# Kernel tuning notes

Measured on AMD Instinct MI355X. Metric: run time of the kernel, lower is better.

Reference implementation:

```python
import jax, jax.numpy as jnp
import numpy as np


def _maxpool2(x):
    # 2x2 max pool, stride 2, NCHW
    return jax.lax.reduce_window(x, -jnp.inf, jax.lax.max, (1, 1, 2, 2), (1, 1, 2, 2), 'VALID')


def _up2(x):
    # bilinear upsample x2 with align_corners=True (matches nn.Upsample), NCHW, separable
    def rs(a, axis):
        n = a.shape[axis]
        out = 2 * n
        c = jnp.arange(out) * ((n - 1) / (out - 1))
        i0 = jnp.floor(c).astype(jnp.int32)
        i1 = jnp.minimum(i0 + 1, n - 1)
        w = (c - i0).astype(a.dtype)
        lo = jnp.take(a, i0, axis=axis)
        hi = jnp.take(a, i1, axis=axis)
        shp = [1] * a.ndim
        shp[axis] = out
        w = w.reshape(shp)
        return lo * (1 - w) + hi * w
    return rs(rs(x, 2), 3)


def _conv_experts(x, w, b):
    # x [B,Cin,H,W], w [E,Cout,Cin,3,3], b [E,Cout] -> [E,B,Cout,H,W]
    def one(we, be):
        y = jax.lax.conv_general_dilated(x, we, (1, 1), 'SAME',
                                         dimension_numbers=('NCHW', 'OIHW', 'NCHW'))
        return jax.nn.relu(y + be[None, :, None, None])
    return jax.vmap(one)(w, b)


def _moe(x, cw, cb, gw, gb, nw, nb, eps, k):
    # noisy top-k gate (create_gate) + fused gated expert sum (eval_gate)
    B = x.shape[0]
    xf = x.reshape(B, -1)
    g = xf @ gw + gb                      # [B,E]
    noise = jax.nn.softplus(xf @ nw + nb)
    g = g + eps[None, :] * noise          # shared per-expert gaussian noise * per-sample scale
    E = g.shape[1]
    if E > 2:
        _, idx = jax.lax.top_k(g.sum(axis=0), k)   # top-k experts by batch-summed gate
        mask = jnp.zeros((E,), bool).at[idx].set(True)
        g = jnp.where(mask[None, :], g, 0.0)       # zero BEFORE softmax, as in the original
    gate = jax.nn.softmax(g, axis=-1)
    y = _conv_experts(x, cw, cb)          # [E,B,C,H,W]
    # collapses the original experts x batch python double-loop into one contraction
    return jnp.einsum('ebchw,be->bchw', y, gate)


def setup_inputs():
    key = jax.random.key(0)
    keys = iter(jax.random.split(key, 40))
    def rn(shape, scale=1.0):
        return jax.random.normal(next(keys), shape, jnp.float32) * scale
    B, W, E = 2048, 10, 4
    inp = {'x': rn((B, 1, 28, 28))}
    conv_shapes = [(E, W, 1, 3, 3), (E, W, W, 3, 3), (E, 2 * W, W, 3, 3),
                   (E, W, 3 * W, 3, 3), (E, W, 2 * W, 3, 3)]
    gate_in = [784, 1960, 490, 5880, 15680]
    for i in range(5):
        inp[f'cw{i+1}'] = rn(conv_shapes[i], 0.1)
        inp[f'cb{i+1}'] = rn((E, conv_shapes[i][1]), 0.1)
        inp[f'gw{i+1}'] = rn((gate_in[i], E), 0.02)
        inp[f'gb{i+1}'] = rn((E,), 0.02)
        inp[f'nw{i+1}'] = rn((gate_in[i], E), 0.02)
        inp[f'nb{i+1}'] = rn((E,), 0.02)
        inp[f'eps{i+1}'] = rn((E,), 1.0)   # N(mu=0, sigma=1) gate noise, fixed for determinism
    inp['wlast'] = rn((1, W, 1, 1), 0.1)
    inp['blast'] = rn((1,), 0.1)
    inp['k'] = 2
    return inp


def reference(x, cw1, cb1, gw1, gb1, nw1, nb1, eps1,
              cw2, cb2, gw2, gb2, nw2, nb2, eps2,
              cw3, cb3, gw3, gb3, nw3, nb3, eps3,
              cw4, cb4, gw4, gb4, nw4, nb4, eps4,
              cw5, cb5, gw5, gb5, nw5, nb5, eps5,
              wlast, blast, k):
    conv1 = _moe(x, cw1, cb1, gw1, gb1, nw1, nb1, eps1, k)        # [B,10,28,28]
    h = _maxpool2(conv1)                                          # [B,10,14,14]
    conv2 = _moe(h, cw2, cb2, gw2, gb2, nw2, nb2, eps2, k)        # [B,10,14,14]
    h = _maxpool2(conv2)                                          # [B,10,7,7]
    conv3 = _moe(h, cw3, cb3, gw3, gb3, nw3, nb3, eps3, k)        # [B,20,7,7]
    h = jnp.concatenate([_up2(conv3), conv2], axis=1)             # [B,30,14,14]
    h = _moe(h, cw4, cb4, gw4, gb4, nw4, nb4, eps4, k)            # [B,10,14,14]
    h = jnp.concatenate([_up2(h), conv1], axis=1)                 # [B,20,28,28]
    h = _moe(h, cw5, cb5, gw5, gb5, nw5, nb5, eps5, k)            # [B,10,28,28]
    out = jnp.einsum('bchw,oc->bohw', h, wlast[:, :, 0, 0]) + blast[None, :, None, None]
    return out
```

## Files before the change

### kernel.cpp

```cpp
#include <hip/hip_runtime.h>
#include <hip/hip_bf16.h>
#include <math.h>


constexpr int BATCH = 2048;

constexpr size_t PADF    = 1024;
constexpr size_t F_CONV1 = (size_t)BATCH * 10 * 784;
constexpr size_t F_XPAD  = (size_t)BATCH * 784;
constexpr size_t F_P1    = (size_t)BATCH * 10 * 196;
constexpr size_t F_CONV2 = F_P1;
constexpr size_t F_P2    = (size_t)BATCH * 10 * 49;
constexpr size_t F_CONV3 = (size_t)BATCH * 20 * 49;
constexpr size_t F_UP3   = (size_t)BATCH * 20 * 196;
constexpr size_t F_M4    = F_P1;
constexpr size_t F_UP4   = F_CONV1;

constexpr size_t O_CONV1 = PADF;
constexpr size_t O_Z2    = O_CONV1 + F_CONV1 + PADF;
constexpr size_t O_XPAD  = O_Z2;
constexpr size_t O_P1    = O_XPAD + F_XPAD + PADF;
constexpr size_t O_CONV2 = O_P1 + F_P1 + PADF;
constexpr size_t O_P2    = O_CONV2 + F_CONV2 + PADF;
constexpr size_t O_CONV3 = O_P2 + F_P2 + PADF;
constexpr size_t O_UP3   = O_CONV3 + F_CONV3 + PADF;
constexpr size_t O_M4    = O_UP3 + F_UP3 + PADF;
constexpr size_t O_UP4   = O_Z2;
constexpr size_t O_GRAW  = O_M4 + F_M4 + PADF;
constexpr size_t O_CS    = O_GRAW + 5 * (size_t)BATCH * 4;
constexpr size_t WS_FLOATS = O_CS + 5 * 64 + PADF;

__device__ __forceinline__ float softplusf(float z) {
    return fmaxf(z, 0.0f) + log1pf(expf(-fabsf(z)));
}

__device__ __forceinline__ float4 ld4(const float* p) {
    return *(const float4*)p;
}

constexpr int cdivc(int a, int b) { return (a + b - 1) / b; }
constexpr int pb4(int H, int W) {
    return cdivc(BATCH * ((H + 3) / 4) * W, 256);
}

template <int C1HW, int C2HW>
__global__ __launch_bounds__(256) void gate_block_v4(
    const float* __restrict__ x1, const float* __restrict__ x2,
    const float* __restrict__ gw, const float* __restrict__ gb,
    const float* __restrict__ nw, const float* __restrict__ nb,
    const float* __restrict__ eps,
    float* __restrict__ graw)
{
    constexpr int DV = (C1HW + C2HW) / 4;
    const int b0  = blockIdx.x * 2;
    const int tid = threadIdx.x;

    float ga[2][4] = {}, na[2][4] = {};

    for (int g = tid; g < DV; g += 256) {
        const int d = g * 4;
        float4 xv[2];
        #pragma unroll
        for (int ss = 0; ss < 2; ++ss) {
            const int b = b0 + ss;
            if constexpr (C2HW > 0) {
                xv[ss] = (d < C1HW) ? ld4(x1 + (size_t)b * C1HW + d)
                                    : ld4(x2 + (size_t)b * C2HW + (d - C1HW));
            } else {
                xv[ss] = ld4(x1 + (size_t)b * C1HW + d);
            }
        }
        #pragma unroll
        for (int j = 0; j < 4; ++j) {
            const float4 gv = ((const float4*)gw)[d + j];
            const float4 nv = ((const float4*)nw)[d + j];
            #pragma unroll
            for (int ss = 0; ss < 2; ++ss) {
                const float val = (&xv[ss].x)[j];
                ga[ss][0] = fmaf(val, gv.x, ga[ss][0]);
                ga[ss][1] = fmaf(val, gv.y, ga[ss][1]);
                ga[ss][2] = fmaf(val, gv.z, ga[ss][2]);
                ga[ss][3] = fmaf(val, gv.w, ga[ss][3]);
                na[ss][0] = fmaf(val, nv.x, na[ss][0]);
                na[ss][1] = fmaf(val, nv.y, na[ss][1]);
                na[ss][2] = fmaf(val, nv.z, na[ss][2]);
                na[ss][3] = fmaf(val, nv.w, na[ss][3]);
            }
        }
    }
    #pragma unroll
    for (int m = 32; m >= 1; m >>= 1) {
        #pragma unroll
        for (int ss = 0; ss < 2; ++ss)
            #pragma unroll
            for (int e = 0; e < 4; ++e) {
                ga[ss][e] += __shfl_xor(ga[ss][e], m, 64);
                na[ss][e] += __shfl_xor(na[ss][e], m, 64);
            }
    }
    __shared__ float red[4][16];
    const int wave = tid >> 6, lane = tid & 63;
    if (lane == 0) {
        #pragma unroll
        for (int ss = 0; ss < 2; ++ss)
            #pragma unroll
            for (int e = 0; e < 4; ++e) {
                red[wave][ss * 8 + e]     = ga[ss][e];
                red[wave][ss * 8 + 4 + e] = na[ss][e];
            }
    }
    __syncthreads();
    if (tid < 2) {
        const int ss = tid;
        #pragma unroll
        for (int e = 0; e < 4; ++e) {
            const float G = red[0][ss*8+e] + red[1][ss*8+e]
                          + red[2][ss*8+e] + red[3][ss*8+e];
            const float N = red[0][ss*8+4+e] + red[1][ss*8+4+e]
                          + red[2][ss*8+4+e] + red[3][ss*8+4+e];
            graw[(b0 + ss) * 4 + e] = G + gb[e] + eps[e] * softplusf(N + nb[e]);
        }
    }
}

template <int D>
__global__ __launch_bounds__(256) void gate_block_s(
    const float* __restrict__ x1,
    const float* __restrict__ gw, const float* __restrict__ gb,
    const float* __restrict__ nw, const float* __restrict__ nb,
    const float* __restrict__ eps,
    float* __restrict__ graw)
{
    const int b   = blockIdx.x;
    const int tid = threadIdx.x;

    float ga0 = 0.f, ga1 = 0.f, ga2 = 0.f, ga3 = 0.f;
    float na0 = 0.f, na1 = 0.f, na2 = 0.f, na3 = 0.f;

    for (int d = tid; d < D; d += 256) {
        const float val = x1[(size_t)b * D + d];
        const float4 gv = ((const float4*)gw)[d];
        const float4 nv = ((const float4*)nw)[d];
        ga0 = fmaf(val, gv.x, ga0); ga1 = fmaf(val, gv.y, ga1);
        ga2 = fmaf(val, gv.z, ga2); ga3 = fmaf(val, gv.w, ga3);
        na0 = fmaf(val, nv.x, na0); na1 = fmaf(val, nv.y, na1);
        na2 = fmaf(val, nv.z, na2); na3 = fmaf(val, nv.w, na3);
    }
    #pragma unroll
    for (int m = 32; m >= 1; m >>= 1) {
        ga0 += __shfl_xor(ga0, m, 64); ga1 += __shfl_xor(ga1, m, 64);
        ga2 += __shfl_xor(ga2, m, 64); ga3 += __shfl_xor(ga3, m, 64);
        na0 += __shfl_xor(na0, m, 64); na1 += __shfl_xor(na1, m, 64);
        na2 += __shfl_xor(na2, m, 64); na3 += __shfl_xor(na3, m, 64);
    }
    __shared__ float red[4][8];
    const int wave = tid >> 6, lane = tid & 63;
    if (lane == 0) {
        red[wave][0] = ga0; red[wave][1] = ga1; red[wave][2] = ga2; red[wave][3] = ga3;
        red[wave][4] = na0; red[wave][5] = na1; red[wave][6] = na2; red[wave][7] = na3;
    }
    __syncthreads();
    if (tid == 0) {
        float G[8];
        #pragma unroll
        for (int i = 0; i < 8; ++i)
            G[i] = red[0][i] + red[1][i] + red[2][i] + red[3][i];
        #pragma unroll
        for (int e = 0; e < 4; ++e) {
            graw[b * 4 + e] = G[e] + gb[e] + eps[e] * softplusf(G[4 + e] + nb[e]);
        }
    }
}

__global__ __launch_bounds__(256) void gate_reduce(
    const float* __restrict__ graw, float* __restrict__ cs)
{
    const int tid = threadIdx.x;
    float a0 = 0.f, a1 = 0.f, a2 = 0.f, a3 = 0.f;
    for (int b = tid; b < BATCH; b += 256) {
        const float4 v = ld4(graw + b * 4);
        a0 += v.x; a1 += v.y; a2 += v.z; a3 += v.w;
    }
    #pragma unroll
    for (int m = 32; m >= 1; m >>= 1) {
        a0 += __shfl_xor(a0, m, 64); a1 += __shfl_xor(a1, m, 64);
        a2 += __shfl_xor(a2, m, 64); a3 += __shfl_xor(a3, m, 64);
    }
    __shared__ float red[4][4];
    const int wave = tid >> 6, lane = tid & 63;
    if (lane == 0) {
        red[wave][0] = a0; red[wave][1] = a1; red[wave][2] = a2; red[wave][3] = a3;
    }
    __syncthreads();
    if (tid < 4) {
        cs[tid] = red[0][tid] + red[1][tid] + red[2][tid] + red[3][tid];
    }
}

__device__ __forceinline__ void gate_final(
    const float* __restrict__ graw, const float* __restrict__ colsum,
    const int* __restrict__ kp, int b, float gt[4])
{
    float cs[4], gr[4];
    #pragma unroll
    for (int e = 0; e < 4; ++e) { cs[e] = colsum[e]; gr[e] = graw[b * 4 + e]; }
    int k = kp[0];
    k = (k < 1) ? 1 : (k > 4 ? 4 : k);
    bool sel[4] = {false, false, false, false};
    for (int it = 0; it < k; ++it) {
        int bi = 0; float bv = -INFINITY;
        #pragma unroll
        for (int e = 0; e < 4; ++e)
            if (!sel[e] && cs[e] > bv) { bv = cs[e]; bi = e; }
        sel[bi] = true;
    }
    float g[4];
    #pragma unroll
    for (int e = 0; e < 4; ++e) g[e] = sel[e] ? gr[e] : 0.0f;
    const float mx = fmaxf(fmaxf(g[0], g[1]), fmaxf(g[2], g[3]));
    const float e0 = expf(g[0] - mx), e1 = expf(g[1] - mx);
    const float e2 = expf(g[2] - mx), e3 = expf(g[3] - mx);
    const float inv = 1.0f / (e0 + e1 + e2 + e3);
    gt[0] = e0 * inv; gt[1] = e1 * inv; gt[2] = e2 * inv; gt[3] = e3 * inv;
}

template <int CIN1, int CIN2, int COUT, int POOL, int FINAL>
__global__ __launch_bounds__(256) void moe_conv_q4(
    const float* __restrict__ x1, const float* __restrict__ x2,
    const float* __restrict__ cw, const float* __restrict__ cb,
    const float* __restrict__ graw, const float* __restrict__ colsum,
    const int* __restrict__ kp,
    float* __restrict__ out, float* __restrict__ pout,
    const float* __restrict__ wl, const float* __restrict__ bl)
{
    constexpr int H = 28, W = 28;
    constexpr int CIN = CIN1 + CIN2;
    constexpr int CG  = 2;
    constexpr int NCG = COUT / CG;
    constexpr int TOTAL = BATCH * 14 * 7;

    __shared__ __align__(16) float wlds[CIN * 72];

    const unsigned bid = blockIdx.x;
    const unsigned xcd = bid & 7u;
    const unsigned sub = bid >> 3;
    const unsigned cg  = sub % NCG;
    const unsigned tl  = sub / NCG;
    const unsigned tile = tl * 8u + xcd;
    const int c0 = (int)cg * CG;

    for (int idx = threadIdx.x; idx < CIN * 72; idx += 256) {
        const int ci = idx / 72;
        const int r  = idx % 72;
        const int k  = r / 8;
        const int je = r % 8;
        wlds[idx] = cw[((size_t)((je & 3) * COUT + c0 + (je >> 2)) * CIN + ci) * 9 + k];
    }
    __syncthreads();

    const int t = (int)tile * 256 + (int)threadIdx.x;
    if (t >= TOTAL) return;
    const int b  = t / 98;
    const int r  = t - b * 98;
    const int hh = r / 7;
    const int q  = r - hh * 7;
    const int h0 = 2 * hh;
    const int w0 = 4 * q;

    float gt[4];
    gate_final(graw, colsum, kp, b, gt);

    const float rt = (h0 > 0)      ? 1.0f : 0.0f;
    const float rb = (h0 + 2 < H)  ? 1.0f : 0.0f;
    const float cl = (w0 > 0)      ? 1.0f : 0.0f;
    const float cr = (w0 + 4 < W)  ? 1.0f : 0.0f;

    float acc[2][4][CG][4];
    #pragma unroll
    for (int j = 0; j < CG; ++j) {
        #pragma unroll
        for (int e = 0; e < 4; ++e) {
            const float bv = cb[e * COUT + c0 + j];
            #pragma unroll
            for (int rr = 0; rr < 2; ++rr)
                #pragma unroll
                for (int p = 0; p < 4; ++p) acc[rr][p][j][e] = bv;
        }
    }

    const int rbase = (h0 - 1) * W + w0;
    const float* xb1 = x1 + (size_t)b * CIN1 * (H * W);
    const float* xb2 = (CIN2 > 0) ? (x2 + (size_t)b * CIN2 * (H * W)) : nullptr;

    auto xplane = [&](int ci) -> const float* {
        if constexpr (CIN2 > 0)
            return (ci < CIN1) ? (xb1 + ci * (H * W)) : (xb2 + (ci - CIN1) * (H * W));
        else
            return xb1 + ci * (H * W);
    };
    auto load_taps = [&](int ci, float v[4][6]) {
        const float* rp = xplane(ci) + rbase;
        #pragma unroll
        for (int rr = 0; rr < 4; ++rr) {
            const float4 c = ld4(rp + rr * W);
            v[rr][0] = rp[rr * W - 1];
            v[rr][1] = c.x; v[rr][2] = c.y; v[rr][3] = c.z; v[rr][4] = c.w;
            v[rr][5] = rp[rr * W + 4];
        }
    };
    auto fma_taps = [&](int ci, const float v[4][6]) {
        float mv[4][6];
        #pragma unroll
        for (int rr = 0; rr < 4; ++rr) {
            #pragma unroll
            for (int c = 0; c < 6; ++c) mv[rr][c] = v[rr][c];
            mv[rr][0] *= cl;
            mv[rr][5] *= cr;
        }
        #pragma unroll
        for (int c = 0; c < 6; ++c) { mv[0][c] *= rt; mv[3][c] *= rb; }

        const float4* wp = (const float4*)&wlds[ci * 72];
        #pragma unroll
        for (int k = 0; k < 9; ++k) {
            const float4 wA = wp[k * 2];
            const float4 wB = wp[k * 2 + 1];
            const int kh = k / 3, kw = k % 3;
            #pragma unroll
            for (int rr = 0; rr < 2; ++rr) {
                #pragma unroll
                for (int p = 0; p < 4; ++p) {
                    const float tap = mv[rr + kh][p + kw];
                    acc[rr][p][0][0] = fmaf(tap, wA.x, acc[rr][p][0][0]);
                    acc[rr][p][0][1] = fmaf(tap, wA.y, acc[rr][p][0][1]);
                    acc[rr][p][0][2] = fmaf(tap, wA.z, acc[rr][p][0][2]);
                    acc[rr][p][0][3] = fmaf(tap, wA.w, acc[rr][p][0][3]);
                    acc[rr][p][1][0] = fmaf(tap, wB.x, acc[rr][p][1][0]);
                    acc[rr][p][1][1] = fmaf(tap, wB.y, acc[rr][p][1][1]);
                    acc[rr][p][1][2] = fmaf(tap, wB.z, acc[rr][p][1][2]);
                    acc[rr][p][1][3] = fmaf(tap, wB.w, acc[rr][p][1][3]);
                }
            }
        }
    };

    float vA[4][6], vB[4][6];
    load_taps(0, vA);
    #pragma unroll 1
    for (int ci = 0; ci + 2 <= CIN; ci += 2) {
        load_taps(ci + 1, vB);
        fma_taps(ci, vA);
        if (ci + 2 < CIN) load_taps(ci + 2, vA);
        fma_taps(ci + 1, vB);
    }
    if constexpr (CIN & 1) {
        fma_taps(CIN - 1, vA);
    }

    float s[2][4][CG];
    #pragma unroll
    for (int rr = 0; rr < 2; ++rr)
        #pragma unroll
        for (int p = 0; p < 4; ++p)
            #pragma unroll
            for (int j = 0; j < CG; ++j)
                s[rr][p][j] = gt[0] * fmaxf(acc[rr][p][j][0], 0.f)
                            + gt[1] * fmaxf(acc[rr][p][j][1], 0.f)
                            + gt[2] * fmaxf(acc[rr][p][j][2], 0.f)
                            + gt[3] * fmaxf(acc[rr][p][j][3], 0.f);

    if constexpr (FINAL) {
        const float w0f = wl[c0], w1f = wl[c0 + 1];
        const float bshare = bl[0] * (1.0f / (float)NCG);
        float* op = out + (size_t)b * (H * W) + h0 * W + w0;
        #pragma unroll
        for (int rr = 0; rr < 2; ++rr)
            #pragma unroll
            for (int p = 0; p < 4; ++p)
                atomicAdd(&op[rr * W + p],
                          s[rr][p][0] * w0f + s[rr][p][1] * w1f + bshare);
    } else {
        #pragma unroll
        for (int j = 0; j < CG; ++j) {
            float* op = out + ((size_t)b * COUT + c0 + j) * (H * W) + h0 * W + w0;
            #pragma unroll
            for (int rr = 0; rr < 2; ++rr) {
                float4 o = {s[rr][0][j], s[rr][1][j], s[rr][2][j], s[rr][3][j]};
                *(float4*)(op + rr * W) = o;
            }
        }
    }

    if constexpr (POOL) {
        constexpr int H2 = 14, W2 = 14;
        #pragma unroll
        for (int j = 0; j < CG; ++j) {
            float2 o;
            o.x = fmaxf(fmaxf(s[0][0][j], s[0][1][j]), fmaxf(s[1][0][j], s[1][1][j]));
            o.y = fmaxf(fmaxf(s[0][2][j], s[0][3][j]), fmaxf(s[1][2][j], s[1][3][j]));
            float* pp = pout + ((size_t)b * COUT + c0 + j) * (H2 * W2)
                        + hh * W2 + (w0 >> 1);
            *(float2*)pp = o;
        }
    }
}

template <int CIN1, int CIN2, int COUT, int H, int W, int POOL>
__global__ __launch_bounds__(256) void moe_conv4(
    const float* __restrict__ x1, const float* __restrict__ x2,
    const float* __restrict__ cw, const float* __restrict__ cb,
    const float* __restrict__ graw, const float* __restrict__ colsum,
    const int* __restrict__ kp,
    float* __restrict__ out, float* __restrict__ pout)
{
    constexpr int CIN = CIN1 + CIN2;
    constexpr int CG  = 2;
    constexpr int NCG = COUT / CG;
    constexpr int HG  = (H + 3) / 4;
    constexpr int TOTAL = BATCH * HG * W;

    __shared__ __align__(16) float wlds[CIN * 72];

    const unsigned bid = blockIdx.x;
    const unsigned xcd = bid & 7u;
    const unsigned sub = bid >> 3;
    const unsigned cg  = sub % NCG;
    const unsigned tl  = sub / NCG;
    const unsigned tile = tl * 8u + xcd;
    const int c0 = (int)cg * CG;

    for (int idx = threadIdx.x; idx < CIN * 72; idx += 256) {
        const int ci = idx / 72;
        const int r  = idx % 72;
        const int k  = r / 8;
        const int je = r % 8;
        wlds[idx] = cw[((size_t)((je & 3) * COUT + c0 + (je >> 2)) * CIN + ci) * 9 + k];
    }
    __syncthreads();

    const int t = (int)tile * 256 + (int)threadIdx.x;
    if (t >= TOTAL) return;
    const int b  = t / (HG * W);
    const int r  = t - b * (HG * W);
    const int hg = r / W;
    const int w  = r - hg * W;
    const int h0 = hg * 4;

    float gt[4];
    gate_final(graw, colsum, kp, b, gt);

    float m[6][3];
    #pragma unroll
    for (int rr = 0; rr < 6; ++rr) {
        const int y = h0 - 1 + rr;
        const float my = (y >= 0 && y < H) ? 1.0f : 0.0f;
        #pragma unroll
        for (int dc = 0; dc < 3; ++dc) {
            const int xx = w - 1 + dc;
            m[rr][dc] = ((xx >= 0 && xx < W) ? 1.0f : 0.0f) * my;
        }
    }
    const int base = (h0 - 1) * W + (w - 1);

    float acc[4][CG][4];
    #pragma unroll
    for (int j = 0; j < CG; ++j) {
        #pragma unroll
        for (int e = 0; e < 4; ++e) {
            const float bv = cb[e * COUT + c0 + j];
            #pragma unroll
            for (int rr = 0; rr < 4; ++rr) acc[rr][j][e] = bv;
        }
    }

    const float* xb1 = x1 + (size_t)b * CIN1 * (H * W);
    const float* xb2 = (CIN2 > 0) ? (x2 + (size_t)b * CIN2 * (H * W)) : nullptr;

    auto xplane = [&](int ci) -> const float* {
        if constexpr (CIN2 > 0)
            return (ci < CIN1) ? (xb1 + ci * (H * W)) : (xb2 + (ci - CIN1) * (H * W));
        else
            return xb1 + ci * (H * W);
    };
    auto load_taps = [&](int ci, float v[6][3]) {
        const float* xp = xplane(ci);
        #pragma unroll
        for (int rr = 0; rr < 6; ++rr)
            #pragma unroll
            for (int dc = 0; dc < 3; ++dc)
                v[rr][dc] = xp[base + rr * W + dc];
    };
    auto fma_taps = [&](int ci, const float v[6][3]) {
        float mv[6][3];
        #pragma unroll
        for (int rr = 0; rr < 6; ++rr)
            #pragma unroll
            for (int dc = 0; dc < 3; ++dc)
                mv[rr][dc] = v[rr][dc] * m[rr][dc];
        const float4* wp = (const float4*)&wlds[ci * 72];
        #pragma unroll
        for (int k = 0; k < 9; ++k) {
            const float4 wA = wp[k * 2];
            const float4 wB = wp[k * 2 + 1];
            const int kh = k / 3, kw = k % 3;
            #pragma unroll
            for (int rr = 0; rr < 4; ++rr) {
                const float tap = mv[rr + kh][kw];
                acc[rr][0][0] = fmaf(tap, wA.x, acc[rr][0][0]);
                acc[rr][0][1] = fmaf(tap, wA.y, acc[rr][0][1]);
                acc[rr][0][2] = fmaf(tap, wA.z, acc[rr][0][2]);
                acc[rr][0][3] = fmaf(tap, wA.w, acc[rr][0][3]);
                acc[rr][1][0] = fmaf(tap, wB.x, acc[rr][1][0]);
                acc[rr][1][1] = fmaf(tap, wB.y, acc[rr][1][1]);
                acc[rr][1][2] = fmaf(tap, wB.z, acc[rr][1][2]);
                acc[rr][1][3] = fmaf(tap, wB.w, acc[rr][1][3]);
            }
        }
    };

    float vA[6][3], vB[6][3];
    load_taps(0, vA);
    #pragma unroll 1
    for (int ci = 0; ci + 2 <= CIN; ci += 2) {
        load_taps(ci + 1, vB);
        fma_taps(ci, vA);
        if (ci + 2 < CIN) load_taps(ci + 2, vA);
        fma_taps(ci + 1, vB);
    }
    if constexpr (CIN & 1) {
        fma_taps(CIN - 1, vA);
    }

    float s[4][CG];
    #pragma unroll
    for (int rr = 0; rr < 4; ++rr)
        #pragma unroll
        for (int j = 0; j < CG; ++j)
            s[rr][j] = gt[0] * fmaxf(acc[rr][j][0], 0.f)
                     + gt[1] * fmaxf(acc[rr][j][1], 0.f)
                     + gt[2] * fmaxf(acc[rr][j][2], 0.f)
                     + gt[3] * fmaxf(acc[rr][j][3], 0.f);

    #pragma unroll
    for (int j = 0; j < CG; ++j) {
        float* op = out + ((size_t)b * COUT + c0 + j) * (H * W) + h0 * W + w;
        #pragma unroll
        for (int rr = 0; rr < 4; ++rr)
            if (h0 + rr < H) op[rr * W] = s[rr][j];
    }

    if constexpr (POOL) {
        constexpr int H2 = H / 2, W2 = W / 2;
        #pragma unroll
        for (int j = 0; j < CG; ++j) {
            float cm0 = fmaxf(s[0][j], s[1][j]);
            float cm1 = fmaxf(s[2][j], s[3][j]);
            const float o0 = fmaxf(cm0, __shfl_xor(cm0, 1, 64));
            const float o1 = fmaxf(cm1, __shfl_xor(cm1, 1, 64));
            if ((w & 1) == 0) {
                const int pr0 = h0 >> 1;
                float* pp = pout + ((size_t)b * COUT + c0 + j) * (H2 * W2) + (w >> 1);
                if (pr0     < H2) pp[pr0 * W2]       = o0;
                if (pr0 + 1 < H2) pp[(pr0 + 1) * W2] = o1;
            }
        }
    }
}

template <int N>
__global__ __launch_bounds__(256) void upsample2(
    const float* __restrict__ in, float* __restrict__ out, int BC)
{
    constexpr int M = 2 * N;
    const int idx = blockIdx.x * 256 + threadIdx.x;
    const int total = BC * M * M;
    if (idx >= total) return;
    const int x = idx % M;
    int tmp = idx / M;
    const int y = tmp % M;
    const int bc = tmp / M;
    const float scale = (float)((double)(N - 1) / (double)(M - 1));
    const float cy = (float)y * scale;
    const float cx = (float)x * scale;
    const int iy0 = (int)floorf(cy);
    const int ix0 = (int)floorf(cx);
    const int iy1 = min(iy0 + 1, N - 1);
    const int ix1 = min(ix0 + 1, N - 1);
    const float wy = cy - (float)iy0;
    const float wx = cx - (float)ix0;
    const float* p = in + (size_t)bc * N * N;
    const float v00 = p[iy0 * N + ix0], v01 = p[iy0 * N + ix1];
    const float v10 = p[iy1 * N + ix0], v11 = p[iy1 * N + ix1];
    const float a0 = v00 * (1.0f - wy) + v10 * wy;
    const float a1 = v01 * (1.0f - wy) + v11 * wy;
    out[idx] = a0 * (1.0f - wx) + a1 * wx;
}

extern "C" void kernel_launch(void* const* d_in, const int* in_sizes, int n_in,
                              void* d_out, int out_size, void* d_ws, size_t ws_size,
                              hipStream_t stream)
{
    const float* x = (const float*)d_in[0];
    const float* cw[5]; const float* cb[5]; const float* gw[5]; const float* gb[5];
    const float* nw[5]; const float* nb[5]; const float* epsv[5];
    for (int l = 0; l < 5; ++l) {
        cw[l]   = (const float*)d_in[1 + 7 * l + 0];
        cb[l]   = (const float*)d_in[1 + 7 * l + 1];
        gw[l]   = (const float*)d_in[1 + 7 * l + 2];
        gb[l]   = (const float*)d_in[1 + 7 * l + 3];
        nw[l]   = (const float*)d_in[1 + 7 * l + 4];
        nb[l]   = (const float*)d_in[1 + 7 * l + 5];
        epsv[l] = (const float*)d_in[1 + 7 * l + 6];
    }
    const float* wlast = (const float*)d_in[36];
    const float* blast = (const float*)d_in[37];
    const int*   kp    = (const int*)d_in[38];
    float* out = (float*)d_out;
    float* ws  = (float*)d_ws;

    float* conv1 = ws + O_CONV1;
    float* xpad  = ws + O_XPAD;
    float* p1    = ws + O_P1;
    float* conv2 = ws + O_CONV2;
    float* p2    = ws + O_P2;
    float* conv3 = ws + O_CONV3;
    float* up3   = ws + O_UP3;
    float* m4    = ws + O_M4;
    float* up4   = ws + O_UP4;
    float* graw[5]; float* cs[5];
    for (int l = 0; l < 5; ++l) {
        graw[l] = ws + O_GRAW + (size_t)l * BATCH * 4;
        cs[l]   = ws + O_CS + (size_t)l * 64;
    }

    hipMemsetAsync(out, 0, (size_t)out_size * sizeof(float), stream);
    hipMemcpyAsync(xpad, x, (size_t)BATCH * 784 * sizeof(float),
                   hipMemcpyDeviceToDevice, stream);

    #define CDIV(a) (((a) + 255) / 256)
    const int gq  = 784 * 5;
    const int g2  = pb4(14, 14) * 5;
    const int g3  = pb4(7, 7)   * 10;
    const int g4  = pb4(14, 14) * 5;
    const int GB2 = BATCH / 2;

    gate_block_v4<784, 0><<<GB2, 256, 0, stream>>>(
        x, nullptr, gw[0], gb[0], nw[0], nb[0], epsv[0], graw[0]);
    gate_reduce<<<1, 256, 0, stream>>>(graw[0], cs[0]);
    moe_conv_q4<1, 0, 10, 1, 0><<<gq, 256, 0, stream>>>(
        xpad, nullptr, cw[0], cb[0], graw[0], cs[0], kp, conv1, p1,
        nullptr, nullptr);

    gate_block_v4<1960, 0><<<GB2, 256, 0, stream>>>(
        p1, nullptr, gw[1], gb[1], nw[1], nb[1], epsv[1], graw[1]);
    gate_reduce<<<1, 256, 0, stream>>>(graw[1], cs[1]);
    moe_conv4<10, 0, 10, 14, 14, 1><<<g2, 256, 0, stream>>>(
        p1, nullptr, cw[1], cb[1], graw[1], cs[1], kp, conv2, p2);

    gate_block_s<490><<<BATCH, 256, 0, stream>>>(
        p2, gw[2], gb[2], nw[2], nb[2], epsv[2], graw[2]);
    gate_reduce<<<1, 256, 0, stream>>>(graw[2], cs[2]);
    moe_conv4<10, 0, 20, 7, 7, 0><<<g3, 256, 0, stream>>>(
        p2, nullptr, cw[2], cb[2], graw[2], cs[2], kp, conv3, nullptr);
    upsample2<7><<<CDIV(BATCH * 20 * 196), 256, 0, stream>>>(conv3, up3, BATCH * 20);

    gate_block_v4<3920, 1960><<<GB2, 256, 0, stream>>>(
        up3, conv2, gw[3], gb[3], nw[3], nb[3], epsv[3], graw[3]);
    gate_reduce<<<1, 256, 0, stream>>>(graw[3], cs[3]);
    moe_conv4<20, 10, 10, 14, 14, 0><<<g4, 256, 0, stream>>>(
        up3, conv2, cw[3], cb[3], graw[3], cs[3], kp, m4, nullptr);
    upsample2<14><<<CDIV(BATCH * 10 * 784), 256, 0, stream>>>(m4, up4, BATCH * 10);

    gate_block_v4<7840, 7840><<<GB2, 256, 0, stream>>>(
        up4, conv1, gw[4], gb[4], nw[4], nb[4], epsv[4], graw[4]);
    gate_reduce<<<1, 256, 0, stream>>>(graw[4], cs[4]);
    moe_conv_q4<10, 10, 10, 0, 1><<<gq, 256, 0, stream>>>(
        up4, conv1, cw[4], cb[4], graw[4], cs[4], kp, out, nullptr,
        wlast, blast);
    #undef CDIV
}
```

Before: 829.2 us.

## Fuse all MoE stages into one persistent cooperative megakernel with grid syncs

Replaces the sequence of separate gate, reduce, conv and upsample launches with one cooperative persistent kernel. Stages are separated by grid.sync and each stage loops over virtual block indices. The per-sample gate softmax is now computed once per layer into a gate buffer instead of being recomputed by every conv thread. The final layer writes per-channel-group partial sums to a buffer that a last pass reduces, which replaces the atomicAdd output and the memset. The trade-offs are the register and occupancy limit set by the largest fused stage, about twenty grid-wide barriers, and a grid capped at 1024 blocks.

```diff
diff --git a/kernel.cpp b/kernel.cpp
--- a/kernel.cpp
+++ b/kernel.cpp
@@ -1,6 +1,9 @@
 #include <hip/hip_runtime.h>
+#include <hip/hip_cooperative_groups.h>
 #include <hip/hip_bf16.h>
 #include <math.h>
+
+namespace cg = cooperative_groups;
 
 
 constexpr int BATCH = 2048;
@@ -15,6 +18,7 @@
 constexpr size_t F_UP3   = (size_t)BATCH * 20 * 196;
 constexpr size_t F_M4    = F_P1;
 constexpr size_t F_UP4   = F_CONV1;
+constexpr size_t F_M5P   = (size_t)5 * BATCH * 784;
 
 constexpr size_t O_CONV1 = PADF;
 constexpr size_t O_Z2    = O_CONV1 + F_CONV1 + PADF;
@@ -26,37 +30,42 @@
 constexpr size_t O_UP3   = O_CONV3 + F_CONV3 + PADF;
 constexpr size_t O_M4    = O_UP3 + F_UP3 + PADF;
 constexpr size_t O_UP4   = O_Z2;
+constexpr size_t O_M5P   = O_Z2 + F_UP4 + PADF;
 constexpr size_t O_GRAW  = O_M4 + F_M4 + PADF;
-constexpr size_t O_CS    = O_GRAW + 5 * (size_t)BATCH * 4;
-constexpr size_t WS_FLOATS = O_CS + 5 * 64 + PADF;
+constexpr size_t O_GATE  = O_GRAW + 5 * (size_t)BATCH * 4 + PADF;
 
 __device__ __forceinline__ float softplusf(float z) {
     return fmaxf(z, 0.0f) + log1pf(expf(-fabsf(z)));
 }
-
-__device__ __forceinline__ float4 ld4(const float* p) {
-    return *(const float4*)p;
-}
-
-constexpr int cdivc(int a, int b) { return (a + b - 1) / b; }
-constexpr int pb4(int H, int W) {
-    return cdivc(BATCH * ((H + 3) / 4) * W, 256);
-}
+__device__ __forceinline__ float4 ld4(const float* p) { return *(const float4*)p; }
+
+struct Params {
+    const float* x;
+    const float* cw[5]; const float* cb[5];
+    const float* gw[5]; const float* gb[5];
+    const float* nw[5]; const float* nb[5];
+    const float* eps[5];
+    const int*   kp;
+    const float* wlast; const float* blast;
+    float* out;
+    float* conv1; float* xpad; float* p1; float* conv2; float* p2;
+    float* conv3; float* up3; float* m4; float* up4; float* m5p;
+    float* graw; float* gate;
+};
+
+__shared__ __align__(16) float wlds[2176];
+__shared__ float sred[4][16];
 
 template <int C1HW, int C2HW>
-__global__ __launch_bounds__(256) void gate_block_v4(
+__device__ __forceinline__ void dev_gate_v4(
     const float* __restrict__ x1, const float* __restrict__ x2,
     const float* __restrict__ gw, const float* __restrict__ gb,
     const float* __restrict__ nw, const float* __restrict__ nb,
-    const float* __restrict__ eps,
-    float* __restrict__ graw)
+    const float* __restrict__ eps, float* __restrict__ graw, int vb, int tid)
 {
     constexpr int DV = (C1HW + C2HW) / 4;
-    const int b0  = blockIdx.x * 2;
-    const int tid = threadIdx.x;
-
+    const int b0 = vb * 2;
     float ga[2][4] = {}, na[2][4] = {};
-
     for (int g = tid; g < DV; g += 256) {
         const int d = g * 4;
         float4 xv[2];
@@ -98,15 +107,15 @@
                 na[ss][e] += __shfl_xor(na[ss][e], m, 64);
             }
     }
-    __shared__ float red[4][16];
+    __syncthreads();
     const int wave = tid >> 6, lane = tid & 63;
     if (lane == 0) {
         #pragma unroll
         for (int ss = 0; ss < 2; ++ss)
             #pragma unroll
             for (int e = 0; e < 4; ++e) {
-                red[wave][ss * 8 + e]     = ga[ss][e];
-                red[wave][ss * 8 + 4 + e] = na[ss][e];
+                sred[wave][ss * 8 + e]     = ga[ss][e];
+                sred[wave][ss * 8 + 4 + e] = na[ss][e];
             }
     }
     __syncthreads();
@@ -114,29 +123,24 @@
         const int ss = tid;
         #pragma unroll
         for (int e = 0; e < 4; ++e) {
-            const float G = red[0][ss*8+e] + red[1][ss*8+e]
-                          + red[2][ss*8+e] + red[3][ss*8+e];
-            const float N = red[0][ss*8+4+e] + red[1][ss*8+4+e]
-                          + red[2][ss*8+4+e] + red[3][ss*8+4+e];
+            const float G = sred[0][ss*8+e] + sred[1][ss*8+e]
+                          + sred[2][ss*8+e] + sred[3][ss*8+e];
+            const float N = sred[0][ss*8+4+e] + sred[1][ss*8+4+e]
+                          + sred[2][ss*8+4+e] + sred[3][ss*8+4+e];
             graw[(b0 + ss) * 4 + e] = G + gb[e] + eps[e] * softplusf(N + nb[e]);
         }
     }
 }
 
 template <int D>
-__global__ __launch_bounds__(256) void gate_block_s(
+__device__ __forceinline__ void dev_gate_s(
     const float* __restrict__ x1,
     const float* __restrict__ gw, const float* __restrict__ gb,
     const float* __restrict__ nw, const float* __restrict__ nb,
-    const float* __restrict__ eps,
-    float* __restrict__ graw)
+    const float* __restrict__ eps, float* __restrict__ graw, int vb, int tid)
 {
-    const int b   = blockIdx.x;
-    const int tid = threadIdx.x;
-
-    float ga0 = 0.f, ga1 = 0.f, ga2 = 0.f, ga3 = 0.f;
-    float na0 = 0.f, na1 = 0.f, na2 = 0.f, na3 = 0.f;
-
+    const int b = vb;
+    float ga0=0,ga1=0,ga2=0,ga3=0,na0=0,na1=0,na2=0,na3=0;
     for (int d = tid; d < D; d += 256) {
         const float val = x1[(size_t)b * D + d];
         const float4 gv = ((const float4*)gw)[d];
@@ -153,32 +157,30 @@
         na0 += __shfl_xor(na0, m, 64); na1 += __shfl_xor(na1, m, 64);
         na2 += __shfl_xor(na2, m, 64); na3 += __shfl_xor(na3, m, 64);
     }
-    __shared__ float red[4][8];
+    __syncthreads();
     const int wave = tid >> 6, lane = tid & 63;
     if (lane == 0) {
-        red[wave][0] = ga0; red[wave][1] = ga1; red[wave][2] = ga2; red[wave][3] = ga3;
-        red[wave][4] = na0; red[wave][5] = na1; red[wave][6] = na2; red[wave][7] = na3;
+        sred[wave][0] = ga0; sred[wave][1] = ga1; sred[wave][2] = ga2; sred[wave][3] = ga3;
+        sred[wave][4] = na0; sred[wave][5] = na1; sred[wave][6] = na2; sred[wave][7] = na3;
     }
     __syncthreads();
     if (tid == 0) {
-        float G[8];
-        #pragma unroll
-        for (int i = 0; i < 8; ++i)
-            G[i] = red[0][i] + red[1][i] + red[2][i] + red[3][i];
         #pragma unroll
         for (int e = 0; e < 4; ++e) {
-            graw[b * 4 + e] = G[e] + gb[e] + eps[e] * softplusf(G[4 + e] + nb[e]);
-        }
-    }
-}
-
-__global__ __launch_bounds__(256) void gate_reduce(
-    const float* __restrict__ graw, float* __restrict__ cs)
+            const float G = sred[0][e]+sred[1][e]+sred[2][e]+sred[3][e];
+            const float N = sred[0][4+e]+sred[1][4+e]+sred[2][4+e]+sred[3][4+e];
+            graw[b * 4 + e] = G + gb[e] + eps[e] * softplusf(N + nb[e]);
+        }
+    }
+}
+
+__device__ __forceinline__ void dev_finalize(
+    const float* __restrict__ graw, const int* __restrict__ kp,
+    float* __restrict__ gate, int tid, int nb)
 {
-    const int tid = threadIdx.x;
-    float a0 = 0.f, a1 = 0.f, a2 = 0.f, a3 = 0.f;
-    for (int b = tid; b < BATCH; b += 256) {
-        const float4 v = ld4(graw + b * 4);
+    float a0=0,a1=0,a2=0,a3=0;
+    for (int i = tid; i < BATCH; i += 256) {
+        const float4 v = ld4(graw + i * 4);
         a0 += v.x; a1 += v.y; a2 += v.z; a3 += v.w;
     }
     #pragma unroll
@@ -186,24 +188,17 @@
         a0 += __shfl_xor(a0, m, 64); a1 += __shfl_xor(a1, m, 64);
         a2 += __shfl_xor(a2, m, 64); a3 += __shfl_xor(a3, m, 64);
     }
-    __shared__ float red[4][4];
+    __syncthreads();
     const int wave = tid >> 6, lane = tid & 63;
     if (lane == 0) {
-        red[wave][0] = a0; red[wave][1] = a1; red[wave][2] = a2; red[wave][3] = a3;
-    }
-    __syncthreads();
-    if (tid < 4) {
-        cs[tid] = red[0][tid] + red[1][tid] + red[2][tid] + red[3][tid];
-    }
-}
-
-__device__ __forceinline__ void gate_final(
-    const float* __restrict__ graw, const float* __restrict__ colsum,
-    const int* __restrict__ kp, int b, float gt[4])
-{
-    float cs[4], gr[4];
-    #pragma unroll
-    for (int e = 0; e < 4; ++e) { cs[e] = colsum[e]; gr[e] = graw[b * 4 + e]; }
+        sred[wave][0] = a0; sred[wave][1] = a1; sred[wave][2] = a2; sred[wave][3] = a3;
+    }
+    __syncthreads();
+    float cs[4];
+    #pragma unroll
+    for (int e = 0; e < 4; ++e)
+        cs[e] = sred[0][e] + sred[1][e] + sred[2][e] + sred[3][e];
+
     int k = kp[0];
     k = (k < 1) ? 1 : (k > 4 ? 4 : k);
     bool sel[4] = {false, false, false, false};
@@ -214,24 +209,28 @@
             if (!sel[e] && cs[e] > bv) { bv = cs[e]; bi = e; }
         sel[bi] = true;
     }
-    float g[4];
-    #pragma unroll
-    for (int e = 0; e < 4; ++e) g[e] = sel[e] ? gr[e] : 0.0f;
-    const float mx = fmaxf(fmaxf(g[0], g[1]), fmaxf(g[2], g[3]));
-    const float e0 = expf(g[0] - mx), e1 = expf(g[1] - mx);
-    const float e2 = expf(g[2] - mx), e3 = expf(g[3] - mx);
-    const float inv = 1.0f / (e0 + e1 + e2 + e3);
-    gt[0] = e0 * inv; gt[1] = e1 * inv; gt[2] = e2 * inv; gt[3] = e3 * inv;
-}
-
-template <int CIN1, int CIN2, int COUT, int POOL, int FINAL>
-__global__ __launch_bounds__(256) void moe_conv_q4(
+    for (int b = blockIdx.x * 256 + tid; b < BATCH; b += nb * 256) {
+        float g[4];
+        #pragma unroll
+        for (int e = 0; e < 4; ++e) {
+            const float v = graw[b * 4 + e];
+            g[e] = sel[e] ? v : 0.0f;
+        }
+        const float mx = fmaxf(fmaxf(g[0], g[1]), fmaxf(g[2], g[3]));
+        const float e0 = expf(g[0]-mx), e1 = expf(g[1]-mx);
+        const float e2 = expf(g[2]-mx), e3 = expf(g[3]-mx);
+        const float inv = 1.0f / (e0 + e1 + e2 + e3);
+        float4 o = {e0*inv, e1*inv, e2*inv, e3*inv};
+        *(float4*)(gate + b * 4) = o;
+    }
+}
+
+template <int CIN1, int CIN2, int COUT, int POOL, int PARTIAL>
+__device__ __forceinline__ void dev_conv_q4(
     const float* __restrict__ x1, const float* __restrict__ x2,
     const float* __restrict__ cw, const float* __restrict__ cb,
-    const float* __restrict__ graw, const float* __restrict__ colsum,
-    const int* __restrict__ kp,
-    float* __restrict__ out, float* __restrict__ pout,
-    const float* __restrict__ wl, const float* __restrict__ bl)
+    const float* __restrict__ gate, const float* __restrict__ wl,
+    float* __restrict__ out, float* __restrict__ pout, int vb, int tid)
 {
     constexpr int H = 28, W = 28;
     constexpr int CIN = CIN1 + CIN2;
@@ -239,17 +238,16 @@
     constexpr int NCG = COUT / CG;
     constexpr int TOTAL = BATCH * 14 * 7;
 
-    __shared__ __align__(16) float wlds[CIN * 72];
-
-    const unsigned bid = blockIdx.x;
+    const unsigned bid = (unsigned)vb;
     const unsigned xcd = bid & 7u;
     const unsigned sub = bid >> 3;
-    const unsigned cg  = sub % NCG;
+    const unsigned cgq = sub % NCG;
     const unsigned tl  = sub / NCG;
     const unsigned tile = tl * 8u + xcd;
-    const int c0 = (int)cg * CG;
-
-    for (int idx = threadIdx.x; idx < CIN * 72; idx += 256) {
+    const int c0 = (int)cgq * CG;
+
+    __syncthreads();
+    for (int idx = tid; idx < CIN * 72; idx += 256) {
         const int ci = idx / 72;
         const int r  = idx % 72;
         const int k  = r / 8;
@@ -258,7 +256,7 @@
     }
     __syncthreads();
 
-    const int t = (int)tile * 256 + (int)threadIdx.x;
+    const int t = (int)tile * 256 + tid;
     if (t >= TOTAL) return;
     const int b  = t / 98;
     const int r  = t - b * 98;
@@ -267,13 +265,13 @@
     const int h0 = 2 * hh;
     const int w0 = 4 * q;
 
-    float gt[4];
-    gate_final(graw, colsum, kp, b, gt);
-
-    const float rt = (h0 > 0)      ? 1.0f : 0.0f;
-    const float rb = (h0 + 2 < H)  ? 1.0f : 0.0f;
-    const float cl = (w0 > 0)      ? 1.0f : 0.0f;
-    const float cr = (w0 + 4 < W)  ? 1.0f : 0.0f;
+    const float4 gv4 = ld4(gate + b * 4);
+    const float gt0 = gv4.x, gt1 = gv4.y, gt2 = gv4.z, gt3 = gv4.w;
+
+    const float rt = (h0 > 0)     ? 1.0f : 0.0f;
+    const float rb = (h0 + 2 < H) ? 1.0f : 0.0f;
+    const float cl = (w0 > 0)     ? 1.0f : 0.0f;
+    const float cr = (w0 + 4 < W) ? 1.0f : 0.0f;
 
     float acc[2][4][CG][4];
     #pragma unroll
@@ -319,7 +317,6 @@
         }
         #pragma unroll
         for (int c = 0; c < 6; ++c) { mv[0][c] *= rt; mv[3][c] *= rb; }
-
         const float4* wp = (const float4*)&wlds[ci * 72];
         #pragma unroll
         for (int k = 0; k < 9; ++k) {
@@ -364,21 +361,22 @@
         for (int p = 0; p < 4; ++p)
             #pragma unroll
             for (int j = 0; j < CG; ++j)
-                s[rr][p][j] = gt[0] * fmaxf(acc[rr][p][j][0], 0.f)
-                            + gt[1] * fmaxf(acc[rr][p][j][1], 0.f)
-                            + gt[2] * fmaxf(acc[rr][p][j][2], 0.f)
-                            + gt[3] * fmaxf(acc[rr][p][j][3], 0.f);
-
-    if constexpr (FINAL) {
+                s[rr][p][j] = gt0 * fmaxf(acc[rr][p][j][0], 0.f)
+                            + gt1 * fmaxf(acc[rr][p][j][1], 0.f)
+                            + gt2 * fmaxf(acc[rr][p][j][2], 0.f)
+                            + gt3 * fmaxf(acc[rr][p][j][3], 0.f);
+
+    if constexpr (PARTIAL) {
         const float w0f = wl[c0], w1f = wl[c0 + 1];
-        const float bshare = bl[0] * (1.0f / (float)NCG);
-        float* op = out + (size_t)b * (H * W) + h0 * W + w0;
-        #pragma unroll
-        for (int rr = 0; rr < 2; ++rr)
-            #pragma unroll
-            for (int p = 0; p < 4; ++p)
-                atomicAdd(&op[rr * W + p],
-                          s[rr][p][0] * w0f + s[rr][p][1] * w1f + bshare);
+        float* op = out + ((size_t)cgq * BATCH + b) * (H * W) + h0 * W + w0;
+        #pragma unroll
+        for (int rr = 0; rr < 2; ++rr) {
+            float4 o = {s[rr][0][0]*w0f + s[rr][0][1]*w1f,
+                        s[rr][1][0]*w0f + s[rr][1][1]*w1f,
+                        s[rr][2][0]*w0f + s[rr][2][1]*w1f,
+                        s[rr][3][0]*w0f + s[rr][3][1]*w1f};
+            *(float4*)(op + rr * W) = o;
+        }
     } else {
         #pragma unroll
         for (int j = 0; j < CG; ++j) {
@@ -406,12 +404,11 @@
 }
 
 template <int CIN1, int CIN2, int COUT, int H, int W, int POOL>
-__global__ __launch_bounds__(256) void moe_conv4(
+__device__ __forceinline__ void dev_conv4(
     const float* __restrict__ x1, const float* __restrict__ x2,
     const float* __restrict__ cw, const float* __restrict__ cb,
-    const float* __restrict__ graw, const float* __restrict__ colsum,
-    const int* __restrict__ kp,
-    float* __restrict__ out, float* __restrict__ pout)
+    const float* __restrict__ gate,
+    float* __restrict__ out, float* __restrict__ pout, int vb, int tid)
 {
     constexpr int CIN = CIN1 + CIN2;
     constexpr int CG  = 2;
@@ -419,17 +416,16 @@
     constexpr int HG  = (H + 3) / 4;
     constexpr int TOTAL = BATCH * HG * W;
 
-    __shared__ __align__(16) float wlds[CIN * 72];
-
-    const unsigned bid = blockIdx.x;
+    const unsigned bid = (unsigned)vb;
     const unsigned xcd = bid & 7u;
     const unsigned sub = bid >> 3;
-    const unsigned cg  = sub % NCG;
+    const unsigned cgq = sub % NCG;
     const unsigned tl  = sub / NCG;
     const unsigned tile = tl * 8u + xcd;
-    const int c0 = (int)cg * CG;
-
-    for (int idx = threadIdx.x; idx < CIN * 72; idx += 256) {
+    const int c0 = (int)cgq * CG;
+
+    __syncthreads();
+    for (int idx = tid; idx < CIN * 72; idx += 256) {
         const int ci = idx / 72;
         const int r  = idx % 72;
         const int k  = r / 8;
@@ -438,7 +434,7 @@
     }
     __syncthreads();
 
-    const int t = (int)tile * 256 + (int)threadIdx.x;
+    const int t = (int)tile * 256 + tid;
     if (t >= TOTAL) return;
     const int b  = t / (HG * W);
     const int r  = t - b * (HG * W);
@@ -446,8 +442,8 @@
     const int w  = r - hg * W;
     const int h0 = hg * 4;
 
-    float gt[4];
-    gate_final(graw, colsum, kp, b, gt);
+    const float4 gv4 = ld4(gate + b * 4);
+    const float gt0 = gv4.x, gt1 = gv4.y, gt2 = gv4.z, gt3 = gv4.w;
 
     float m[6][3];
     #pragma unroll
@@ -488,15 +484,9 @@
         for (int rr = 0; rr < 6; ++rr)
             #pragma unroll
             for (int dc = 0; dc < 3; ++dc)
-                v[rr][dc] = xp[base + rr * W + dc];
+                v[rr][dc] = xp[base + rr * W + dc] * m[rr][dc];
     };
     auto fma_taps = [&](int ci, const float v[6][3]) {
-        float mv[6][3];
-        #pragma unroll
-        for (int rr = 0; rr < 6; ++rr)
-            #pragma unroll
-            for (int dc = 0; dc < 3; ++dc)
-                mv[rr][dc] = v[rr][dc] * m[rr][dc];
         const float4* wp = (const float4*)&wlds[ci * 72];
         #pragma unroll
         for (int k = 0; k < 9; ++k) {
@@ -505,7 +495,7 @@
             const int kh = k / 3, kw = k % 3;
             #pragma unroll
             for (int rr = 0; rr < 4; ++rr) {
-                const float tap = mv[rr + kh][kw];
+                const float tap = v[rr + kh][kw];
                 acc[rr][0][0] = fmaf(tap, wA.x, acc[rr][0][0]);
                 acc[rr][0][1] = fmaf(tap, wA.y, acc[rr][0][1]);
                 acc[rr][0][2] = fmaf(tap, wA.z, acc[rr][0][2]);
@@ -536,10 +526,10 @@
     for (int rr = 0; rr < 4; ++rr)
         #pragma unroll
         for (int j = 0; j < CG; ++j)
-            s[rr][j] = gt[0] * fmaxf(acc[rr][j][0], 0.f)
-                     + gt[1] * fmaxf(acc[rr][j][1], 0.f)
-                     + gt[2] * fmaxf(acc[rr][j][2], 0.f)
-                     + gt[3] * fmaxf(acc[rr][j][3], 0.f);
+            s[rr][j] = gt0 * fmaxf(acc[rr][j][0], 0.f)
+                     + gt1 * fmaxf(acc[rr][j][1], 0.f)
+                     + gt2 * fmaxf(acc[rr][j][2], 0.f)
+                     + gt3 * fmaxf(acc[rr][j][3], 0.f);
 
     #pragma unroll
     for (int j = 0; j < CG; ++j) {
@@ -568,114 +558,170 @@
 }
 
 template <int N>
-__global__ __launch_bounds__(256) void upsample2(
-    const float* __restrict__ in, float* __restrict__ out, int BC)
+__device__ __forceinline__ void dev_up2(
+    const float* __restrict__ in, float* __restrict__ out, int BC,
+    int gid, int stride)
 {
     constexpr int M = 2 * N;
-    const int idx = blockIdx.x * 256 + threadIdx.x;
     const int total = BC * M * M;
-    if (idx >= total) return;
-    const int x = idx % M;
-    int tmp = idx / M;
-    const int y = tmp % M;
-    const int bc = tmp / M;
     const float scale = (float)((double)(N - 1) / (double)(M - 1));
-    const float cy = (float)y * scale;
-    const float cx = (float)x * scale;
-    const int iy0 = (int)floorf(cy);
-    const int ix0 = (int)floorf(cx);
-    const int iy1 = min(iy0 + 1, N - 1);
-    const int ix1 = min(ix0 + 1, N - 1);
-    const float wy = cy - (float)iy0;
-    const float wx = cx - (float)ix0;
-    const float* p = in + (size_t)bc * N * N;
-    const float v00 = p[iy0 * N + ix0], v01 = p[iy0 * N + ix1];
-    const float v10 = p[iy1 * N + ix0], v11 = p[iy1 * N + ix1];
-    const float a0 = v00 * (1.0f - wy) + v10 * wy;
-    const float a1 = v01 * (1.0f - wy) + v11 * wy;
-    out[idx] = a0 * (1.0f - wx) + a1 * wx;
+    for (int idx = gid; idx < total; idx += stride) {
+        const int x = idx % M;
+        int tmp = idx / M;
+        const int y = tmp % M;
+        const int bc = tmp / M;
+        const float cy = (float)y * scale;
+        const float cx = (float)x * scale;
+        const int iy0 = (int)floorf(cy);
+        const int ix0 = (int)floorf(cx);
+        const int iy1 = min(iy0 + 1, N - 1);
+        const int ix1 = min(ix0 + 1, N - 1);
+        const float wy = cy - (float)iy0;
+        const float wx = cx - (float)ix0;
+        const float* p = in + (size_t)bc * N * N;
+        const float v00 = p[iy0 * N + ix0], v01 = p[iy0 * N + ix1];
+        const float v10 = p[iy1 * N + ix0], v11 = p[iy1 * N + ix1];
+        const float a0 = v00 * (1.0f - wy) + v10 * wy;
+        const float a1 = v01 * (1.0f - wy) + v11 * wy;
+        out[idx] = a0 * (1.0f - wx) + a1 * wx;
+    }
+}
+
+__global__ void __launch_bounds__(256) meganet(Params P) {
+    cg::grid_group grid = cg::this_grid();
+    const int tid = threadIdx.x;
+    const int nb  = (int)gridDim.x;
+    const int gid = (int)blockIdx.x * 256 + tid;
+    const int gstride = nb * 256;
+
+    float* graw[5]; float* gate[5];
+    #pragma unroll
+    for (int l = 0; l < 5; ++l) {
+        graw[l] = P.graw + (size_t)l * BATCH * 4;
+        gate[l] = P.gate + (size_t)l * BATCH * 4;
+    }
+
+    for (int i = gid; i < BATCH * 784; i += gstride) P.xpad[i] = P.x[i];
+    grid.sync();
+
+    for (int vb = blockIdx.x; vb < 1024; vb += nb)
+        dev_gate_v4<784, 0>(P.x, nullptr, P.gw[0], P.gb[0], P.nw[0], P.nb[0],
+                            P.eps[0], graw[0], vb, tid);
+    grid.sync();
+    dev_finalize(graw[0], P.kp, gate[0], tid, nb);
+    grid.sync();
+    for (int vb = blockIdx.x; vb < 3920; vb += nb)
+        dev_conv_q4<1, 0, 10, 1, 0>(P.xpad, nullptr, P.cw[0], P.cb[0],
+                                    gate[0], nullptr, P.conv1, P.p1, vb, tid);
+    grid.sync();
+
+    for (int vb = blockIdx.x; vb < 1024; vb += nb)
+        dev_gate_v4<1960, 0>(P.p1, nullptr, P.gw[1], P.gb[1], P.nw[1], P.nb[1],
+                             P.eps[1], graw[1], vb, tid);
+    grid.sync();
+    dev_finalize(graw[1], P.kp, gate[1], tid, nb);
+    grid.sync();
+    for (int vb = blockIdx.x; vb < 2240; vb += nb)
+        dev_conv4<10, 0, 10, 14, 14, 1>(P.p1, nullptr, P.cw[1], P.cb[1],
+                                        gate[1], P.conv2, P.p2, vb, tid);
+    grid.sync();
+
+    for (int vb = blockIdx.x; vb < 2048; vb += nb)
+        dev_gate_s<490>(P.p2, P.gw[2], P.gb[2], P.nw[2], P.nb[2],
+                        P.eps[2], graw[2], vb, tid);
+    grid.sync();
+    dev_finalize(graw[2], P.kp, gate[2], tid, nb);
+    grid.sync();
+    for (int vb = blockIdx.x; vb < 1120; vb += nb)
+        dev_conv4<10, 0, 20, 7, 7, 0>(P.p2, nullptr, P.cw[2], P.cb[2],
+                                      gate[2], P.conv3, nullptr, vb, tid);
+    grid.sync();
+    dev_up2<7>(P.conv3, P.up3, BATCH * 20, gid, gstride);
+    grid.sync();
+
+    for (int vb = blockIdx.x; vb < 1024; vb += nb)
+        dev_gate_v4<3920, 1960>(P.up3, P.conv2, P.gw[3], P.gb[3], P.nw[3], P.nb[3],
+                                P.eps[3], graw[3], vb, tid);
+    grid.sync();
+    dev_finalize(graw[3], P.kp, gate[3], tid, nb);
+    grid.sync();
+    for (int vb = blockIdx.x; vb < 2240; vb += nb)
+        dev_conv4<20, 10, 10, 14, 14, 0>(P.up3, P.conv2, P.cw[3], P.cb[3],
+                                         gate[3], P.m4, nullptr, vb, tid);
+    grid.sync();
+    dev_up2<14>(P.m4, P.up4, BATCH * 10, gid, gstride);
+    grid.sync();
+
+    for (int vb = blockIdx.x; vb < 1024; vb += nb)
+        dev_gate_v4<7840, 7840>(P.up4, P.conv1, P.gw[4], P.gb[4], P.nw[4], P.nb[4],
+                                P.eps[4], graw[4], vb, tid);
+    grid.sync();
+    dev_finalize(graw[4], P.kp, gate[4], tid, nb);
+    grid.sync();
+    for (int vb = blockIdx.x; vb < 3920; vb += nb)
+        dev_conv_q4<10, 10, 10, 0, 1>(P.up4, P.conv1, P.cw[4], P.cb[4],
+                                      gate[4], P.wlast, P.m5p, nullptr, vb, tid);
+    grid.sync();
+
+    {
+        const float bias = P.blast[0];
+        const int total4 = BATCH * 196;
+        for (int i = gid; i < total4; i += gstride) {
+            const int b = i / 196;
+            const int s4 = i % 196;
+            float4 acc = {bias, bias, bias, bias};
+            #pragma unroll
+            for (int cgq = 0; cgq < 5; ++cgq) {
+                const float4 v = ld4(P.m5p + ((size_t)cgq * BATCH + b) * 784 + s4 * 4);
+                acc.x += v.x; acc.y += v.y; acc.z += v.z; acc.w += v.w;
+            }
+            ((float4*)P.out)[i] = acc;
+        }
+    }
 }
 
 extern "C" void kernel_launch(void* const* d_in, const int* in_sizes, int n_in,
                               void* d_out, int out_size, void* d_ws, size_t ws_size,
                               hipStream_t stream)
 {
-    const float* x = (const float*)d_in[0];
-    const float* cw[5]; const float* cb[5]; const float* gw[5]; const float* gb[5];
-    const float* nw[5]; const float* nb[5]; const float* epsv[5];
+    Params P;
+    P.x = (const float*)d_in[0];
     for (int l = 0; l < 5; ++l) {
-        cw[l]   = (const float*)d_in[1 + 7 * l + 0];
-        cb[l]   = (const float*)d_in[1 + 7 * l + 1];
-        gw[l]   = (const float*)d_in[1 + 7 * l + 2];
-        gb[l]   = (const float*)d_in[1 + 7 * l + 3];
-        nw[l]   = (const float*)d_in[1 + 7 * l + 4];
-        nb[l]   = (const float*)d_in[1 + 7 * l + 5];
-        epsv[l] = (const float*)d_in[1 + 7 * l + 6];
-    }
-    const float* wlast = (const float*)d_in[36];
-    const float* blast = (const float*)d_in[37];
-    const int*   kp    = (const int*)d_in[38];
-    float* out = (float*)d_out;
-    float* ws  = (float*)d_ws;
-
-    float* conv1 = ws + O_CONV1;
-    float* xpad  = ws + O_XPAD;
-    float* p1    = ws + O_P1;
-    float* conv2 = ws + O_CONV2;
-    float* p2    = ws + O_P2;
-    float* conv3 = ws + O_CONV3;
-    float* up3   = ws + O_UP3;
-    float* m4    = ws + O_M4;
-    float* up4   = ws + O_UP4;
-    float* graw[5]; float* cs[5];
-    for (int l = 0; l < 5; ++l) {
-        graw[l] = ws + O_GRAW + (size_t)l * BATCH * 4;
-        cs[l]   = ws + O_CS + (size_t)l * 64;
-    }
-
-    hipMemsetAsync(out, 0, (size_t)out_size * sizeof(float), stream);
-    hipMemcpyAsync(xpad, x, (size_t)BATCH * 784 * sizeof(float),
-                   hipMemcpyDeviceToDevice, stream);
-
-    #define CDIV(a) (((a) + 255) / 256)
-    const int gq  = 784 * 5;
-    const int g2  = pb4(14, 14) * 5;
-    const int g3  = pb4(7, 7)   * 10;
-    const int g4  = pb4(14, 14) * 5;
-    const int GB2 = BATCH / 2;
-
-    gate_block_v4<784, 0><<<GB2, 256, 0, stream>>>(
-        x, nullptr, gw[0], gb[0], nw[0], nb[0], epsv[0], graw[0]);
-    gate_reduce<<<1, 256, 0, stream>>>(graw[0], cs[0]);
-    moe_conv_q4<1, 0, 10, 1, 0><<<gq, 256, 0, stream>>>(
-        xpad, nullptr, cw[0], cb[0], graw[0], cs[0], kp, conv1, p1,
-        nullptr, nullptr);
-
-    gate_block_v4<1960, 0><<<GB2, 256, 0, stream>>>(
-        p1, nullptr, gw[1], gb[1], nw[1], nb[1], epsv[1], graw[1]);
-    gate_reduce<<<1, 256, 0, stream>>>(graw[1], cs[1]);
-    moe_conv4<10, 0, 10, 14, 14, 1><<<g2, 256, 0, stream>>>(
-        p1, nullptr, cw[1], cb[1], graw[1], cs[1], kp, conv2, p2);
-
-    gate_block_s<490><<<BATCH, 256, 0, stream>>>(
-        p2, gw[2], gb[2], nw[2], nb[2], epsv[2], graw[2]);
-    gate_reduce<<<1, 256, 0, stream>>>(graw[2], cs[2]);
-    moe_conv4<10, 0, 20, 7, 7, 0><<<g3, 256, 0, stream>>>(
-        p2, nullptr, cw[2], cb[2], graw[2], cs[2], kp, conv3, nullptr);
-    upsample2<7><<<CDIV(BATCH * 20 * 196), 256, 0, stream>>>(conv3, up3, BATCH * 20);
-
-    gate_block_v4<3920, 1960><<<GB2, 256, 0, stream>>>(
-        up3, conv2, gw[3], gb[3], nw[3], nb[3], epsv[3], graw[3]);
-    gate_reduce<<<1, 256, 0, stream>>>(graw[3], cs[3]);
-    moe_conv4<20, 10, 10, 14, 14, 0><<<g4, 256, 0, stream>>>(
-        up3, conv2, cw[3], cb[3], graw[3], cs[3], kp, m4, nullptr);
-    upsample2<14><<<CDIV(BATCH * 10 * 784), 256, 0, stream>>>(m4, up4, BATCH * 10);
-
-    gate_block_v4<7840, 7840><<<GB2, 256, 0, stream>>>(
-        up4, conv1, gw[4], gb[4], nw[4], nb[4], epsv[4], graw[4]);
-    gate_reduce<<<1, 256, 0, stream>>>(graw[4], cs[4]);
-    moe_conv_q4<10, 10, 10, 0, 1><<<gq, 256, 0, stream>>>(
-        up4, conv1, cw[4], cb[4], graw[4], cs[4], kp, out, nullptr,
-        wlast, blast);
-    #undef CDIV
-}
+        P.cw[l]  = (const float*)d_in[1 + 7 * l + 0];
+        P.cb[l]  = (const float*)d_in[1 + 7 * l + 1];
+        P.gw[l]  = (const float*)d_in[1 + 7 * l + 2];
+        P.gb[l]  = (const float*)d_in[1 + 7 * l + 3];
+        P.nw[l]  = (const float*)d_in[1 + 7 * l + 4];
+        P.nb[l]  = (const float*)d_in[1 + 7 * l + 5];
+        P.eps[l] = (const float*)d_in[1 + 7 * l + 6];
+    }
+    P.wlast = (const float*)d_in[36];
+    P.blast = (const float*)d_in[37];
+    P.kp    = (const int*)d_in[38];
+    P.out   = (float*)d_out;
+
+    float* ws = (float*)d_ws;
+    P.conv1 = ws + O_CONV1;
+    P.xpad  = ws + O_XPAD;
+    P.p1    = ws + O_P1;
+    P.conv2 = ws + O_CONV2;
+    P.p2    = ws + O_P2;
+    P.conv3 = ws + O_CONV3;
+    P.up3   = ws + O_UP3;
+    P.m4    = ws + O_M4;
+    P.up4   = ws + O_UP4;
+    P.m5p   = ws + O_M5P;
+    P.graw  = ws + O_GRAW;
+    P.gate  = ws + O_GATE;
+
+    int maxB = 0;
+    hipOccupancyMaxActiveBlocksPerMultiprocessor(
+        &maxB, reinterpret_cast<const void*>(&meganet), 256, 0);
+    if (maxB < 1) maxB = 1;
+    int grid = maxB * 256;
+    if (grid > 1024) grid = 1024;
+
+    void* args[] = {(void*)&P};
+    hipLaunchCooperativeKernel(reinterpret_cast<const void*>(&meganet),
+                               dim3(grid), dim3(256), args, 0, stream);
+}
```

After: 1.531 ms. 1.85x slower.
